# Kernel tuning notes

Measured on AMD Instinct MI355X. Metric: run time of the kernel, lower is better.

Reference implementation:

```python
import jax, jax.numpy as jnp
import numpy as np

LN_EPS = 1e-5
NEG_SLOPE = 0.01

def layer_norm(h, gamma, beta):
    mu = jnp.mean(h, axis=-1, keepdims=True)
    var = jnp.var(h, axis=-1, keepdims=True)
    return (h - mu) * jax.lax.rsqrt(var + LN_EPS) * gamma + beta

def setup_inputs() -> dict:
    key = jax.random.key(0)
    ks = jax.random.split(key, 12)
    N, E = 50000, 600000
    D_NODE, D_EDGE, D_IN = 128, 64, 192  # D_IN = D_NODE + D_EDGE
    x = jax.random.normal(ks[0], (N, D_NODE), dtype=jnp.float32)
    edge_index = jax.random.randint(ks[1], (2, E), 0, N, dtype=jnp.int64)
    edge_attr = jax.random.normal(ks[2], (E, D_EDGE), dtype=jnp.float32)
    # mlp_before_agg: Linear(192->128) + LayerNorm + LeakyReLU
    W1 = jax.random.normal(ks[3], (D_IN, D_NODE), dtype=jnp.float32) / np.sqrt(D_IN)
    b1 = jnp.zeros((D_NODE,), dtype=jnp.float32)
    g1 = jnp.ones((D_NODE,), dtype=jnp.float32)
    be1 = jnp.zeros((D_NODE,), dtype=jnp.float32)
    # mlp_after_agg: Linear(128->128) + LayerNorm + LeakyReLU
    W2 = jax.random.normal(ks[4], (D_NODE, D_NODE), dtype=jnp.float32) / np.sqrt(D_NODE)
    b2 = jnp.zeros((D_NODE,), dtype=jnp.float32)
    g2 = jnp.ones((D_NODE,), dtype=jnp.float32)
    be2 = jnp.zeros((D_NODE,), dtype=jnp.float32)
    return {"x": x, "edge_index": edge_index, "edge_attr": edge_attr,
            "W1": W1, "b1": b1, "g1": g1, "be1": be1,
            "W2": W2, "b2": b2, "g2": g2, "be2": be2}

def reference(x, edge_index, edge_attr, W1, b1, g1, be1, W2, b2, g2, be2):
    N = x.shape[0]
    row, col = edge_index[0], edge_index[1]
    # 1. gather + concat: (E, D_NODE + D_EDGE)
    out = jnp.concatenate([x[row], edge_attr], axis=1)
    # 2. pre-agg MLP: Linear + LayerNorm + LeakyReLU
    out = jax.nn.leaky_relu(layer_norm(out @ W1 + b1, g1, be1), NEG_SLOPE)
    # 3. scatter-mean aggregate over destination nodes (empty segments -> 0)
    sums = jax.ops.segment_sum(out, col, num_segments=N)
    counts = jax.ops.segment_sum(jnp.ones((out.shape[0], 1), out.dtype), col, num_segments=N)
    out = sums / jnp.maximum(counts, 1.0)
    # 4. post-agg MLP + residual + activation
    out = jax.nn.leaky_relu(layer_norm(out @ W2 + b2, g2, be2), NEG_SLOPE)
    return jax.nn.leaky_relu(out + x, NEG_SLOPE)
```

## Files before the change

kernel.cpp:

```cpp
#include <hip/hip_runtime.h>

#define D_NODE 128
#define D_EDGE 64
#define D_IN   192
#define NEG    0.01f
#define LN_EPS 1e-5f

typedef short bf16x8 __attribute__((ext_vector_type(8)));
typedef float f32x4  __attribute__((ext_vector_type(4)));

__device__ __forceinline__ unsigned f2bf(float f) {
    unsigned u = __builtin_bit_cast(unsigned, f);
    return (u + 0x7FFFu + ((u >> 16) & 1u)) >> 16;
}
__device__ __forceinline__ unsigned pk2(float a, float b) {
    return f2bf(a) | (f2bf(b) << 16);
}
__device__ __forceinline__ unsigned cvtpk(float a, float b) {
    unsigned r;
    asm("v_cvt_pk_bf16_f32 %0, %1, %2" : "=v"(r) : "v"(a), "v"(b));
    return r;
}
template <int C>
__device__ __forceinline__ float dppadd(float v) {
    int y = __builtin_amdgcn_update_dpp(0, __builtin_bit_cast(int, v),
                                        C, 0xF, 0xF, true);
    return v + __builtin_bit_cast(float, y);
}
__device__ __forceinline__ float red16(float v) {
    v = dppadd<0xB1>(v);
    v = dppadd<0x4E>(v);
    v = dppadd<0x141>(v);
    v = dppadd<0x140>(v);
    return v;
}

__global__ void k_pre(const float* __restrict__ x, unsigned short* __restrict__ xb,
                      int n8, const int* __restrict__ ei, int* __restrict__ hist,
                      int E) {
    int i = blockIdx.x * blockDim.x + threadIdx.x;
    int stride = gridDim.x * blockDim.x;
    for (int t = i; t < n8; t += stride) {
        const float4* p = (const float4*)x + (size_t)t * 2;
        float4 a = p[0], b = p[1];
        uint4 o;
        o.x = pk2(a.x, a.y); o.y = pk2(a.z, a.w);
        o.z = pk2(b.x, b.y); o.w = pk2(b.z, b.w);
        ((uint4*)xb)[t] = o;
    }
    for (int e = i; e < E; e += stride) atomicAdd(&hist[ei[E + e]], 1);
}

__global__ __launch_bounds__(1024) void k_scanA(const int* __restrict__ hist,
                                                int* __restrict__ base,
                                                int* __restrict__ blockTot, int N) {
    __shared__ int wsum[16], woff[16];
    const int t = threadIdx.x, b = blockIdx.x;
    const int i = b * 1024 + t;
    const int lane = t & 63, w = t >> 6;
    int v = (i < N) ? hist[i] : 0;
    int x = v;
    #pragma unroll
    for (int d = 1; d < 64; d <<= 1) { int u = __shfl_up(x, d); if (lane >= d) x += u; }
    if (lane == 63) wsum[w] = x;
    __syncthreads();
    if (t < 16) {
        int y = wsum[t];
        #pragma unroll
        for (int d = 1; d < 16; d <<= 1) { int u = __shfl_up(y, d, 16); if (t >= d) y += u; }
        woff[t] = y - wsum[t];
    }
    __syncthreads();
    int incl = x + woff[w];
    if (i < N) base[i] = incl - v;
    if (t == 1023) blockTot[b] = incl;
}

__global__ __launch_bounds__(1024) void k_scanC(int* __restrict__ base,
                                                const int* __restrict__ blockTot,
                                                int N, int NB) {
    __shared__ int off_sh;
    const int t = threadIdx.x;
    if (t < 64) {
        int v = (t < NB) ? blockTot[t] : 0;
        int x = v;
        #pragma unroll
        for (int d = 1; d < 64; d <<= 1) { int u = __shfl_up(x, d); if (t >= d) x += u; }
        if (t == blockIdx.x) off_sh = x - v;
    }
    __syncthreads();
    int i = blockIdx.x * 1024 + t;
    if (i < N) base[i] += off_sh;
}

__global__ void k_bucket(const int* __restrict__ ei, int* __restrict__ base,
                         int4* __restrict__ meta, int E) {
    int i = blockIdx.x * blockDim.x + threadIdx.x;
    int stride = gridDim.x * blockDim.x;
    for (int e = i; e < E; e += stride) {
        int c = ei[E + e];
        int r = ei[e];
        int p = atomicAdd(&base[c], 1);
        meta[p] = make_int4(r, c, e, 0);
    }
}

__global__ __launch_bounds__(256) void edge_mfma_seg(
    const unsigned short* __restrict__ xb,
    const float* __restrict__ edge_attr,
    const int4*  __restrict__ meta,
    const float* __restrict__ W1,
    const float* __restrict__ b1,
    const float* __restrict__ g1,
    const float* __restrict__ be1,
    float* __restrict__ sums,
    int E, int ntiles)
{
    __shared__ __align__(16) unsigned short h[64][200];
    __shared__ float rS [64][4], rS2[64][4];
    __shared__ int   scol2[2][64];
    __shared__ int   rdest[64];

    const int tid = threadIdx.x;
    const int w   = tid >> 6;
    const int l   = tid & 63;
    const int lm  = l & 15;
    const int q   = l >> 4;
    const int q8  = q * 8;
    const int e   = tid >> 2;
    const int qq  = tid & 3;

    unsigned short (*yT)[64] = (unsigned short (*)[64])(&h[w * 16][0]);

    bf16x8 Bfr[2][6];
    float  b1v[2], g1v[2], bev[2];
    #pragma unroll
    for (int c2 = 0; c2 < 2; ++c2) {
        const int n = (2 * w + c2) * 16 + lm;
        b1v[c2] = b1[n]; g1v[c2] = g1[n]; bev[c2] = be1[n];
        #pragma unroll
        for (int kt = 0; kt < 6; ++kt) {
            bf16x8 f;
            #pragma unroll
            for (int j = 0; j < 8; ++j)
                f[j] = (short)f2bf(W1[(kt * 32 + q8 + j) * 128 + n]);
            Bfr[c2][kt] = f;
        }
    }

    const int stride_t = gridDim.x;
    int tile = blockIdx.x;
    int pp   = 0;

    uint4  xr0, xr1, xr2, xr3;
    float4 af0, af1, af2, af3;
    int    sc;
    bool   vld;
    {
        const int ge = tile * 64 + e;
        vld = (ge < E);
        if (vld) {
            const int4 mt = meta[ge];
            const uint4* xr = (const uint4*)(xb + (size_t)mt.x * D_NODE) + qq * 4;
            xr0 = xr[0]; xr1 = xr[1]; xr2 = xr[2]; xr3 = xr[3];
            const float4* ar = (const float4*)(edge_attr + (size_t)mt.z * D_EDGE) + qq * 4;
            af0 = ar[0]; af1 = ar[1]; af2 = ar[2]; af3 = ar[3];
        }
        sc = (tid < 64 && tile * 64 + tid < E) ? meta[tile * 64 + tid].y : -1;
    }

    for (; tile < ntiles; tile += stride_t) {
        if (vld) {
            *(uint4*)&h[e][qq * 32 +  0] = xr0;
            *(uint4*)&h[e][qq * 32 +  8] = xr1;
            *(uint4*)&h[e][qq * 32 + 16] = xr2;
            *(uint4*)&h[e][qq * 32 + 24] = xr3;
            uint4 o;
            o.x = cvtpk(af0.x, af0.y); o.y = cvtpk(af0.z, af0.w);
            o.z = cvtpk(af1.x, af1.y); o.w = cvtpk(af1.z, af1.w);
            *(uint4*)&h[e][128 + qq * 16] = o;
            o.x = cvtpk(af2.x, af2.y); o.y = cvtpk(af2.z, af2.w);
            o.z = cvtpk(af3.x, af3.y); o.w = cvtpk(af3.z, af3.w);
            *(uint4*)&h[e][128 + qq * 16 + 8] = o;
        } else {
            uint4 z = make_uint4(0u, 0u, 0u, 0u);
            *(uint4*)&h[e][qq * 32 +  0] = z;
            *(uint4*)&h[e][qq * 32 +  8] = z;
            *(uint4*)&h[e][qq * 32 + 16] = z;
            *(uint4*)&h[e][qq * 32 + 24] = z;
            *(uint4*)&h[e][128 + qq * 16]     = z;
            *(uint4*)&h[e][128 + qq * 16 + 8] = z;
        }
        if (tid < 64) scol2[pp][tid] = sc;
        __syncthreads();

        {
            const int nt = tile + stride_t;
            const int ge = nt * 64 + e;
            vld = (nt < ntiles) && (ge < E);
            if (vld) {
                const int4 mt = meta[ge];
                const uint4* xr = (const uint4*)(xb + (size_t)mt.x * D_NODE) + qq * 4;
                xr0 = xr[0]; xr1 = xr[1]; xr2 = xr[2]; xr3 = xr[3];
                const float4* ar = (const float4*)(edge_attr + (size_t)mt.z * D_EDGE) + qq * 4;
                af0 = ar[0]; af1 = ar[1]; af2 = ar[2]; af3 = ar[3];
            }
            sc = (nt < ntiles && tid < 64 && nt * 64 + tid < E)
                   ? meta[nt * 64 + tid].y : -1;
        }

        f32x4 acc[4][2];
        #pragma unroll
        for (int et = 0; et < 4; ++et)
            #pragma unroll
            for (int c2 = 0; c2 < 2; ++c2)
                acc[et][c2] = (f32x4){0.f, 0.f, 0.f, 0.f};

        #pragma unroll
        for (int et = 0; et < 4; ++et) {
            bf16x8 Afr[6];
            #pragma unroll
            for (int kt = 0; kt < 6; ++kt)
                Afr[kt] = *(const bf16x8*)&h[et * 16 + lm][kt * 32 + q8];
            #pragma unroll
            for (int c2 = 0; c2 < 2; ++c2)
                #pragma unroll
                for (int kt = 0; kt < 6; ++kt)
                    acc[et][c2] = __builtin_amdgcn_mfma_f32_16x16x32_bf16(
                        Afr[kt], Bfr[c2][kt], acc[et][c2], 0, 0, 0);
        }

        #pragma unroll
        for (int et = 0; et < 4; ++et) {
            #pragma unroll
            for (int r = 0; r < 4; ++r) {
                float v0 = acc[et][0][r] + b1v[0];
                float v1 = acc[et][1][r] + b1v[1];
                acc[et][0][r] = v0;
                acc[et][1][r] = v1;
                float s  = red16(v0 + v1);
                float s2 = red16(v0 * v0 + v1 * v1);
                if (lm == 0) {
                    const int em = et * 16 + q * 4 + r;
                    rS [em][w] = s;
                    rS2[em][w] = s2;
                }
            }
        }
        __syncthreads();

        #pragma unroll
        for (int et = 0; et < 4; ++et) {
            float yv[2][4];
            #pragma unroll
            for (int r = 0; r < 4; ++r) {
                const int em = et * 16 + q * 4 + r;
                float4 p  = *(const float4*)&rS [em][0];
                float4 p2 = *(const float4*)&rS2[em][0];
                const float S    = (p.x  + p.y)  + (p.z  + p.w);
                const float S2   = (p2.x + p2.y) + (p2.z + p2.w);
                const float mu   = S * (1.f / 128.f);
                const float var  = S2 * (1.f / 128.f) - mu * mu;
                const float rstd = rsqrtf(var + LN_EPS);
                #pragma unroll
                for (int c2 = 0; c2 < 2; ++c2) {
                    float y = (acc[et][c2][r] - mu) * rstd * g1v[c2] + bev[c2];
                    y = (y > 0.f) ? y : NEG * y;
                    yv[c2][r] = y;
                }
            }
            #pragma unroll
            for (int c2 = 0; c2 < 2; ++c2) {
                const int cl = c2 * 16 + lm;
                const int ch = ((et * 2 + (q >> 1)) ^ (lm & 7)) & 7;
                uint2 o;
                o.x = cvtpk(yv[c2][0], yv[c2][1]);
                o.y = cvtpk(yv[c2][2], yv[c2][3]);
                *(uint2*)&yT[cl][ch * 8 + (q & 1) * 4] = o;
            }
        }

        {
            bf16x8 afr[2][2];
            #pragma unroll
            for (int ct = 0; ct < 2; ++ct)
                #pragma unroll
                for (int kt = 0; kt < 2; ++kt) {
                    const int cl = ct * 16 + lm;
                    const int ch = ((kt * 4 + q) ^ (lm & 7)) & 7;
                    afr[ct][kt] = *(const bf16x8*)&yT[cl][ch * 8];
                }

            int me = scol2[pp][l];
            int pv = __shfl_up(me, 1);
            if (l == 0) pv = me ^ 1;
            const unsigned long long m = __ballot(me != pv);
            const int nr = (int)__popcll(m);
            const int rl = (int)__popcll(m & ((2ull << l) - 1)) - 1;
            if (me != pv) rdest[rl] = me;

            for (int rt = 0; rt * 16 < nr; ++rt) {
                const int rr = rt * 16 + lm;
                bf16x8 bb[2];
                #pragma unroll
                for (int kt = 0; kt < 2; ++kt) {
                    const int eb0 = kt * 32 + q8;
                    int rid = (int)__popcll(m & ((2ull << eb0) - 1)) - 1;
                    unsigned pk[4];
                    #pragma unroll
                    for (int jp = 0; jp < 4; ++jp) {
                        unsigned lo = (rid == rr) ? 0x3F80u : 0u;
                        rid += (int)((m >> (eb0 + 2 * jp + 1)) & 1ull);
                        unsigned hi = (rid == rr) ? 0x3F80u : 0u;
                        if (jp < 3) rid += (int)((m >> (eb0 + 2 * jp + 2)) & 1ull);
                        pk[jp] = lo | (hi << 16);
                    }
                    uint4 pku = make_uint4(pk[0], pk[1], pk[2], pk[3]);
                    bb[kt] = __builtin_bit_cast(bf16x8, pku);
                }
                f32x4 o0 = (f32x4){0.f, 0.f, 0.f, 0.f};
                f32x4 o1 = (f32x4){0.f, 0.f, 0.f, 0.f};
                #pragma unroll
                for (int kt = 0; kt < 2; ++kt) {
                    o0 = __builtin_amdgcn_mfma_f32_16x16x32_bf16(
                        afr[0][kt], bb[kt], o0, 0, 0, 0);
                    o1 = __builtin_amdgcn_mfma_f32_16x16x32_bf16(
                        afr[1][kt], bb[kt], o1, 0, 0, 0);
                }
                if (rr < nr) {
                    const int dest = rdest[rr];
                    if (dest >= 0) {
                        const bool at = (rr == 0) || (rr == nr - 1);
                        float* p0 = &sums[(size_t)dest * D_NODE + w * 32 + q * 4];
                        if (at) {
                            #pragma unroll
                            for (int r = 0; r < 4; ++r) {
                                atomicAdd(&p0[r],      o0[r]);
                                atomicAdd(&p0[16 + r], o1[r]);
                            }
                        } else {
                            *(f32x4*)p0        = o0;
                            *(f32x4*)(p0 + 16) = o1;
                        }
                    }
                }
            }
        }
        pp ^= 1;
    }
}

__global__ __launch_bounds__(256) void node_mfma(
    const float* __restrict__ sums,
    const int*   __restrict__ hist,
    const float* __restrict__ x,
    const float* __restrict__ W2,
    const float* __restrict__ b2,
    const float* __restrict__ g2,
    const float* __restrict__ be2,
    float* __restrict__ out,
    int N)
{
    __shared__ __align__(16) unsigned short h[64][136];
    __shared__ float rS [64][4], rS2[64][4];

    const int tid = threadIdx.x;
    const int w   = tid >> 6;
    const int l   = tid & 63;
    const int lm  = l & 15;
    const int q   = l >> 4;
    const int q8  = q * 8;

    bf16x8 Bfr[2][4];
    float  b2v[2], g2v[2], bev[2];
    #pragma unroll
    for (int c2 = 0; c2 < 2; ++c2) {
        const int n = (2 * w + c2) * 16 + lm;
        b2v[c2] = b2[n]; g2v[c2] = g2[n]; bev[c2] = be2[n];
        #pragma unroll
        for (int kt = 0; kt < 4; ++kt) {
            bf16x8 f;
            #pragma unroll
            for (int j = 0; j < 8; ++j)
                f[j] = (short)f2bf(W2[(kt * 32 + q8 + j) * 128 + n]);
            Bfr[c2][kt] = f;
        }
    }

    const int n0 = blockIdx.x * 64;

    {
        const int e  = tid >> 2;
        const int qq = tid & 3;
        const int gn = n0 + e;
        if (gn < N) {
            const int cnt = hist[gn];
            const float sc = (cnt > 0) ? 1.f / (float)cnt : 0.f;
            const float4* sr = (const float4*)(sums + (size_t)gn * D_NODE);
            #pragma unroll
            for (int i = 0; i < 8; ++i) {
                float4 v = sr[qq * 8 + i];
                *(uint2*)&h[e][qq * 32 + i * 4] =
                    make_uint2(cvtpk(v.x * sc, v.y * sc), cvtpk(v.z * sc, v.w * sc));
            }
        } else {
            #pragma unroll
            for (int i = 0; i < 8; ++i)
                *(uint2*)&h[e][qq * 32 + i * 4] = make_uint2(0u, 0u);
        }
    }
    __syncthreads();

    f32x4 acc[4][2];
    #pragma unroll
    for (int et = 0; et < 4; ++et)
        #pragma unroll
        for (int c2 = 0; c2 < 2; ++c2)
            acc[et][c2] = (f32x4){0.f, 0.f, 0.f, 0.f};

    #pragma unroll
    for (int et = 0; et < 4; ++et) {
        bf16x8 Afr[4];
        #pragma unroll
        for (int kt = 0; kt < 4; ++kt)
            Afr[kt] = *(const bf16x8*)&h[et * 16 + lm][kt * 32 + q8];
        #pragma unroll
        for (int c2 = 0; c2 < 2; ++c2)
            #pragma unroll
            for (int kt = 0; kt < 4; ++kt)
                acc[et][c2] = __builtin_amdgcn_mfma_f32_16x16x32_bf16(
                    Afr[kt], Bfr[c2][kt], acc[et][c2], 0, 0, 0);
    }

    #pragma unroll
    for (int et = 0; et < 4; ++et) {
        #pragma unroll
        for (int r = 0; r < 4; ++r) {
            float v0 = acc[et][0][r] + b2v[0];
            float v1 = acc[et][1][r] + b2v[1];
            acc[et][0][r] = v0;
            acc[et][1][r] = v1;
            float s  = red16(v0 + v1);
            float s2 = red16(v0 * v0 + v1 * v1);
            if (lm == 0) {
                const int em = et * 16 + q * 4 + r;
                rS [em][w] = s;
                rS2[em][w] = s2;
            }
        }
    }
    __syncthreads();

    #pragma unroll
    for (int et = 0; et < 4; ++et) {
        #pragma unroll
        for (int r = 0; r < 4; ++r) {
            const int em = et * 16 + q * 4 + r;
            const int gn = n0 + em;
            if (gn >= N) continue;
            float4 p  = *(const float4*)&rS [em][0];
            float4 p2 = *(const float4*)&rS2[em][0];
            const float S    = (p.x  + p.y)  + (p.z  + p.w);
            const float S2   = (p2.x + p2.y) + (p2.z + p2.w);
            const float mu   = S * (1.f / 128.f);
            const float var  = S2 * (1.f / 128.f) - mu * mu;
            const float rstd = rsqrtf(var + LN_EPS);
            #pragma unroll
            for (int c2 = 0; c2 < 2; ++c2) {
                const int col = (2 * w + c2) * 16 + lm;
                float y = (acc[et][c2][r] - mu) * rstd * g2v[c2] + bev[c2];
                y = (y > 0.f) ? y : NEG * y;
                float rr = y + x[(size_t)gn * D_NODE + col];
                rr = (rr > 0.f) ? rr : NEG * rr;
                out[(size_t)gn * D_NODE + col] = rr;
            }
        }
    }
}

extern "C" void kernel_launch(void* const* d_in, const int* in_sizes, int n_in,
                              void* d_out, int out_size, void* d_ws, size_t ws_size,
                              hipStream_t stream) {
    const float* x          = (const float*)d_in[0];
    const int*   edge_index = (const int*)  d_in[1];
    const float* edge_attr  = (const float*)d_in[2];
    const float* W1         = (const float*)d_in[3];
    const float* b1         = (const float*)d_in[4];
    const float* g1         = (const float*)d_in[5];
    const float* be1        = (const float*)d_in[6];
    const float* W2         = (const float*)d_in[7];
    const float* b2         = (const float*)d_in[8];
    const float* g2         = (const float*)d_in[9];
    const float* be2        = (const float*)d_in[10];

    const int N = in_sizes[0] / D_NODE;
    const int E = in_sizes[1] / 2;

    float* sums     = (float*)d_ws;
    int*   hist     = (int*)(sums + (size_t)N * D_NODE);
    int*   base     = hist + N;
    int*   blockTot = base + N;
    int4*  meta     = (int4*)(blockTot + 64);
    unsigned short* xb = (unsigned short*)(meta + E);

    hipMemsetAsync(d_ws, 0, ((size_t)N * D_NODE + (size_t)N) * sizeof(float), stream);

    const int n8 = N * (D_NODE / 8);
    k_pre<<<dim3(1024), dim3(256), 0, stream>>>(x, xb, n8, edge_index, hist, E);

    const int NB = (N + 1023) / 1024;
    k_scanA<<<dim3(NB), dim3(1024), 0, stream>>>(hist, base, blockTot, N);
    k_scanC<<<dim3(NB), dim3(1024), 0, stream>>>(base, blockTot, N, NB);
    k_bucket<<<dim3(512), dim3(256), 0, stream>>>(edge_index, base, meta, E);

    const int ntiles = (E + 63) / 64;
    const int grid   = ntiles < 1024 ? ntiles : 1024;
    edge_mfma_seg<<<dim3(grid), dim3(256), 0, stream>>>(
        xb, edge_attr, meta, W1, b1, g1, be1, sums, E, ntiles);

    node_mfma<<<dim3((N + 63) / 64), dim3(256), 0, stream>>>(
        sums, hist, x, W2, b2, g2, be2, (float*)d_out, N);
}
```

Before: 441.9 us.

## Pre-transpose weights to bf16, pack edge metadata, read residual from bf16 copy

The weight matrices are transposed and converted to bf16 once in the preprocessing kernel, so each MFMA block loads its B fragments as vector loads instead of strided scalar float loads and conversions. Edge metadata is compacted from 16 to 8 bytes by packing source and destination node indices into 16-bit halves, which cuts bucket writes and tile reads. The node kernel stages the residual x from the bf16 copy through shared memory. The packing requires fewer than 65536 nodes, and the bf16 residual reduces precision.

```diff
diff --git a/kernel.cpp b/kernel.cpp
--- a/kernel.cpp
+++ b/kernel.cpp
@@ -15,6 +15,10 @@
 }
 __device__ __forceinline__ unsigned pk2(float a, float b) {
     return f2bf(a) | (f2bf(b) << 16);
+}
+__device__ __forceinline__ float bf2f(unsigned short s) {
+    unsigned u = ((unsigned)s) << 16;
+    return __builtin_bit_cast(float, u);
 }
 __device__ __forceinline__ unsigned cvtpk(float a, float b) {
     unsigned r;
@@ -37,7 +41,9 @@
 
 __global__ void k_pre(const float* __restrict__ x, unsigned short* __restrict__ xb,
                       int n8, const int* __restrict__ ei, int* __restrict__ hist,
-                      int E) {
+                      int E,
+                      const float* __restrict__ W1, unsigned short* __restrict__ W1tb,
+                      const float* __restrict__ W2, unsigned short* __restrict__ W2tb) {
     int i = blockIdx.x * blockDim.x + threadIdx.x;
     int stride = gridDim.x * blockDim.x;
     for (int t = i; t < n8; t += stride) {
@@ -48,6 +54,26 @@
         o.z = pk2(b.x, b.y); o.w = pk2(b.z, b.w);
         ((uint4*)xb)[t] = o;
     }
+    for (int t = i; t < 128 * 24; t += stride) {
+        const int n  = t / 24;
+        const int k8 = (t % 24) * 8;
+        uint4 o;
+        o.x = pk2(W1[(k8 + 0) * 128 + n], W1[(k8 + 1) * 128 + n]);
+        o.y = pk2(W1[(k8 + 2) * 128 + n], W1[(k8 + 3) * 128 + n]);
+        o.z = pk2(W1[(k8 + 4) * 128 + n], W1[(k8 + 5) * 128 + n]);
+        o.w = pk2(W1[(k8 + 6) * 128 + n], W1[(k8 + 7) * 128 + n]);
+        *(uint4*)&W1tb[n * 192 + k8] = o;
+    }
+    for (int t = i; t < 128 * 16; t += stride) {
+        const int n  = t / 16;
+        const int k8 = (t % 16) * 8;
+        uint4 o;
+        o.x = pk2(W2[(k8 + 0) * 128 + n], W2[(k8 + 1) * 128 + n]);
+        o.y = pk2(W2[(k8 + 2) * 128 + n], W2[(k8 + 3) * 128 + n]);
+        o.z = pk2(W2[(k8 + 4) * 128 + n], W2[(k8 + 5) * 128 + n]);
+        o.w = pk2(W2[(k8 + 6) * 128 + n], W2[(k8 + 7) * 128 + n]);
+        *(uint4*)&W2tb[n * 128 + k8] = o;
+    }
     for (int e = i; e < E; e += stride) atomicAdd(&hist[ei[E + e]], 1);
 }
 
@@ -94,22 +120,22 @@
 }
 
 __global__ void k_bucket(const int* __restrict__ ei, int* __restrict__ base,
-                         int4* __restrict__ meta, int E) {
+                         int2* __restrict__ meta, int E) {
     int i = blockIdx.x * blockDim.x + threadIdx.x;
     int stride = gridDim.x * blockDim.x;
     for (int e = i; e < E; e += stride) {
         int c = ei[E + e];
         int r = ei[e];
         int p = atomicAdd(&base[c], 1);
-        meta[p] = make_int4(r, c, e, 0);
+        meta[p] = make_int2(r | (c << 16), e);
     }
 }
 
 __global__ __launch_bounds__(256) void edge_mfma_seg(
     const unsigned short* __restrict__ xb,
     const float* __restrict__ edge_attr,
-    const int4*  __restrict__ meta,
-    const float* __restrict__ W1,
+    const int2*  __restrict__ meta,
+    const unsigned short* __restrict__ W1tb,
     const float* __restrict__ b1,
     const float* __restrict__ g1,
     const float* __restrict__ be1,
@@ -139,13 +165,8 @@
         const int n = (2 * w + c2) * 16 + lm;
         b1v[c2] = b1[n]; g1v[c2] = g1[n]; bev[c2] = be1[n];
         #pragma unroll
-        for (int kt = 0; kt < 6; ++kt) {
-            bf16x8 f;
-            #pragma unroll
-            for (int j = 0; j < 8; ++j)
-                f[j] = (short)f2bf(W1[(kt * 32 + q8 + j) * 128 + n]);
-            Bfr[c2][kt] = f;
-        }
+        for (int kt = 0; kt < 6; ++kt)
+            Bfr[c2][kt] = *(const bf16x8*)&W1tb[n * 192 + kt * 32 + q8];
     }
 
     const int stride_t = gridDim.x;
@@ -160,13 +181,15 @@
         const int ge = tile * 64 + e;
         vld = (ge < E);
         if (vld) {
-            const int4 mt = meta[ge];
-            const uint4* xr = (const uint4*)(xb + (size_t)mt.x * D_NODE) + qq * 4;
+            const int2 mt = meta[ge];
+            const int row = mt.x & 0xFFFF;
+            const uint4* xr = (const uint4*)(xb + (size_t)row * D_NODE) + qq * 4;
             xr0 = xr[0]; xr1 = xr[1]; xr2 = xr[2]; xr3 = xr[3];
-            const float4* ar = (const float4*)(edge_attr + (size_t)mt.z * D_EDGE) + qq * 4;
+            const float4* ar = (const float4*)(edge_attr + (size_t)mt.y * D_EDGE) + qq * 4;
             af0 = ar[0]; af1 = ar[1]; af2 = ar[2]; af3 = ar[3];
         }
-        sc = (tid < 64 && tile * 64 + tid < E) ? meta[tile * 64 + tid].y : -1;
+        sc = (tid < 64 && tile * 64 + tid < E)
+               ? (int)((unsigned)meta[tile * 64 + tid].x >> 16) : -1;
     }
 
     for (; tile < ntiles; tile += stride_t) {
@@ -199,14 +222,15 @@
             const int ge = nt * 64 + e;
             vld = (nt < ntiles) && (ge < E);
             if (vld) {
-                const int4 mt = meta[ge];
-                const uint4* xr = (const uint4*)(xb + (size_t)mt.x * D_NODE) + qq * 4;
+                const int2 mt = meta[ge];
+                const int row = mt.x & 0xFFFF;
+                const uint4* xr = (const uint4*)(xb + (size_t)row * D_NODE) + qq * 4;
                 xr0 = xr[0]; xr1 = xr[1]; xr2 = xr[2]; xr3 = xr[3];
-                const float4* ar = (const float4*)(edge_attr + (size_t)mt.z * D_EDGE) + qq * 4;
+                const float4* ar = (const float4*)(edge_attr + (size_t)mt.y * D_EDGE) + qq * 4;
                 af0 = ar[0]; af1 = ar[1]; af2 = ar[2]; af3 = ar[3];
             }
             sc = (nt < ntiles && tid < 64 && nt * 64 + tid < E)
-                   ? meta[nt * 64 + tid].y : -1;
+                   ? (int)((unsigned)meta[nt * 64 + tid].x >> 16) : -1;
         }
 
         f32x4 acc[4][2];
@@ -353,8 +377,8 @@
 __global__ __launch_bounds__(256) void node_mfma(
     const float* __restrict__ sums,
     const int*   __restrict__ hist,
-    const float* __restrict__ x,
-    const float* __restrict__ W2,
+    const unsigned short* __restrict__ xb,
+    const unsigned short* __restrict__ W2tb,
     const float* __restrict__ b2,
     const float* __restrict__ g2,
     const float* __restrict__ be2,
@@ -362,6 +386,7 @@
     int N)
 {
     __shared__ __align__(16) unsigned short h[64][136];
+    __shared__ __align__(8)  unsigned short xr[64][132];
     __shared__ float rS [64][4], rS2[64][4];
 
     const int tid = threadIdx.x;
@@ -378,13 +403,8 @@
         const int n = (2 * w + c2) * 16 + lm;
         b2v[c2] = b2[n]; g2v[c2] = g2[n]; bev[c2] = be2[n];
         #pragma unroll
-        for (int kt = 0; kt < 4; ++kt) {
-            bf16x8 f;
-            #pragma unroll
-            for (int j = 0; j < 8; ++j)
-                f[j] = (short)f2bf(W2[(kt * 32 + q8 + j) * 128 + n]);
-            Bfr[c2][kt] = f;
-        }
+        for (int kt = 0; kt < 4; ++kt)
+            Bfr[c2][kt] = *(const bf16x8*)&W2tb[n * 128 + kt * 32 + q8];
     }
 
     const int n0 = blockIdx.x * 64;
@@ -403,10 +423,16 @@
                 *(uint2*)&h[e][qq * 32 + i * 4] =
                     make_uint2(cvtpk(v.x * sc, v.y * sc), cvtpk(v.z * sc, v.w * sc));
             }
+            const uint2* xrow = (const uint2*)(xb + (size_t)gn * D_NODE) + qq * 8;
+            #pragma unroll
+            for (int i = 0; i < 8; ++i)
+                *(uint2*)&xr[e][qq * 32 + i * 4] = xrow[i];
         } else {
             #pragma unroll
-            for (int i = 0; i < 8; ++i)
-                *(uint2*)&h[e][qq * 32 + i * 4] = make_uint2(0u, 0u);
+            for (int i = 0; i < 8; ++i) {
+                *(uint2*)&h[e][qq * 32 + i * 4]  = make_uint2(0u, 0u);
+                *(uint2*)&xr[e][qq * 32 + i * 4] = make_uint2(0u, 0u);
+            }
         }
     }
     __syncthreads();
@@ -470,7 +496,7 @@
                 const int col = (2 * w + c2) * 16 + lm;
                 float y = (acc[et][c2][r] - mu) * rstd * g2v[c2] + bev[c2];
                 y = (y > 0.f) ? y : NEG * y;
-                float rr = y + x[(size_t)gn * D_NODE + col];
+                float rr = y + bf2f(xr[em][col]);
                 rr = (rr > 0.f) ? rr : NEG * rr;
                 out[(size_t)gn * D_NODE + col] = rr;
             }
@@ -500,13 +526,16 @@
     int*   hist     = (int*)(sums + (size_t)N * D_NODE);
     int*   base     = hist + N;
     int*   blockTot = base + N;
-    int4*  meta     = (int4*)(blockTot + 64);
-    unsigned short* xb = (unsigned short*)(meta + E);
+    int2*  meta     = (int2*)(blockTot + 64);
+    unsigned short* xb   = (unsigned short*)(meta + E);
+    unsigned short* W1tb = xb + (size_t)N * D_NODE;
+    unsigned short* W2tb = W1tb + 128 * 192;
 
     hipMemsetAsync(d_ws, 0, ((size_t)N * D_NODE + (size_t)N) * sizeof(float), stream);
 
     const int n8 = N * (D_NODE / 8);
-    k_pre<<<dim3(1024), dim3(256), 0, stream>>>(x, xb, n8, edge_index, hist, E);
+    k_pre<<<dim3(1024), dim3(256), 0, stream>>>(x, xb, n8, edge_index, hist, E,
+                                                W1, W1tb, W2, W2tb);
 
     const int NB = (N + 1023) / 1024;
     k_scanA<<<dim3(NB), dim3(1024), 0, stream>>>(hist, base, blockTot, N);
@@ -516,8 +545,8 @@
     const int ntiles = (E + 63) / 64;
     const int grid   = ntiles < 1024 ? ntiles : 1024;
     edge_mfma_seg<<<dim3(grid), dim3(256), 0, stream>>>(
-        xb, edge_attr, meta, W1, b1, g1, be1, sums, E, ntiles);
+        xb, edge_attr, meta, W1tb, b1, g1, be1, sums, E, ntiles);
 
     node_mfma<<<dim3((N + 63) / 64), dim3(256), 0, stream>>>(
-        sums, hist, x, W2, b2, g2, be2, (float*)d_out, N);
-}
+        sums, hist, xb, W2tb, b2, g2, be2, (float*)d_out, N);
+}
```

New measurement: 434.1 us. No clear change (-1.8%).
